# Performance work log

Hardware: AMD Instinct MI355X
Metric: run time of the kernel (lower is better)

## Reference

```python
import jax, jax.numpy as jnp
import numpy as np

N_NODES = 30000
N_EDGES = 300000
NUM_GRAPHS = 512
HID = 600
IN_FEATS = 9
NUM_TASKS = 128


def setup_inputs() -> dict:
    key = jax.random.key(0)
    ks = jax.random.split(key, 20)
    s = 0.05  # small init scale to keep activations bounded over 5 layers
    inp = {
        'x': jax.random.normal(ks[0], (N_NODES, IN_FEATS), jnp.float32),
        'edge_index': jax.random.randint(ks[1], (2, N_EDGES), 0, N_NODES, jnp.int64),
        'batch_ind': jnp.sort(jax.random.randint(ks[2], (N_NODES,), 0, NUM_GRAPHS, jnp.int64)),
        'w1_0': jax.random.normal(ks[3], (IN_FEATS, HID), jnp.float32) * s,
        'b1_0': jax.random.normal(ks[4], (HID,), jnp.float32) * s,
        'w2_0': jax.random.normal(ks[5], (HID, HID), jnp.float32) * s,
        'b2_0': jax.random.normal(ks[6], (HID,), jnp.float32) * s,
        'w1_r': jax.random.normal(ks[7], (4, HID, HID), jnp.float32) * s,
        'b1_r': jax.random.normal(ks[8], (4, HID), jnp.float32) * s,
        'w2_r': jax.random.normal(ks[9], (4, HID, HID), jnp.float32) * s,
        'b2_r': jax.random.normal(ks[10], (4, HID), jnp.float32) * s,
        'cw1': jax.random.normal(ks[11], (HID, 256), jnp.float32) * s,
        'cb1': jax.random.normal(ks[12], (256,), jnp.float32) * s,
        'cw2': jax.random.normal(ks[13], (256, 256), jnp.float32) * s,
        'cb2': jax.random.normal(ks[14], (256,), jnp.float32) * s,
        'cw3': jax.random.normal(ks[15], (256, NUM_TASKS), jnp.float32) * s,
        'cb3': jax.random.normal(ks[16], (NUM_TASKS,), jnp.float32) * s,
    }
    return inp


def _gin_conv(h, edge_index, w1, b1, w2, b2):
    # sum-aggregate neighbor features: messages flow src -> dst
    msgs = h[edge_index[0]]                                   # [E, d] gather
    agg = jax.ops.segment_sum(msgs, edge_index[1], num_segments=N_NODES)
    z = h + agg                                               # (1 + eps) * x + agg, eps = 0
    z = jax.nn.relu(z @ w1 + b1) @ w2 + b2                    # per-layer MLP [in, 600, 600]
    return z


def _forward(x, edge_index, batch_ind, w1_0, b1_0, w2_0, b2_0,
             w1_r, b1_r, w2_r, b2_r, cw1, cb1, cw2, cb2, cw3, cb3):
    h = _gin_conv(x, edge_index, w1_0, b1_0, w2_0, b2_0)
    h = jax.nn.relu(h)  # inter-layer activation (dropout is identity in eval)
    for i in range(4):  # layers 1..4 (fixed, structurally distinct params)
        h = _gin_conv(h, edge_index, w1_r[i], b1_r[i], w2_r[i], b2_r[i])
        if i < 3:
            h = jax.nn.relu(h)  # no act/dropout after final GNN layer (jk=None)
    feats = jax.ops.segment_sum(h, batch_ind, num_segments=NUM_GRAPHS)  # global_add_pool
    z = jax.nn.relu(feats @ cw1 + cb1)
    z = jax.nn.relu(z @ cw2 + cb2)
    return z @ cw3 + cb3  # [NUM_GRAPHS, NUM_TASKS]


def reference(x, edge_index, batch_ind, w1_0, b1_0, w2_0, b2_0,
              w1_r, b1_r, w2_r, b2_r, cw1, cb1, cw2, cb2, cw3, cb3):
    return _forward(x, edge_index, batch_ind, w1_0, b1_0, w2_0, b2_0,
                    w1_r, b1_r, w2_r, b2_r, cw1, cb1, cw2, cb2, cw3, cb3)
```

## Files before the change

### kernel.cpp

```cpp
#include <hip/hip_runtime.h>

#define N_NODES 30000
#define N_EDGES 300000
#define NUM_GRAPHS 512
#define HID 600
#define IN_FEATS 9
#define NUM_TASKS 128

#define MPAD 30080
#define HPAD 640
#define K0PAD 32

typedef __attribute__((ext_vector_type(4))) float f32x4;
typedef __attribute__((ext_vector_type(8))) short bf16x8;


__device__ __forceinline__ float bflo(unsigned int v) {
  union { unsigned int u; float f; } c; c.u = v << 16; return c.f;
}
__device__ __forceinline__ float bfhi(unsigned int v) {
  union { unsigned int u; float f; } c; c.u = v & 0xffff0000u; return c.f;
}
__device__ __forceinline__ unsigned short f2bf(float f) {
  union { float f; unsigned int u; } c; c.f = f;
  unsigned int u = c.u;
  return (unsigned short)((u + 0x7fffu + ((u >> 16) & 1u)) >> 16);
}
__device__ __forceinline__ unsigned int pack2(float a, float b) {
  return (unsigned int)f2bf(a) | ((unsigned int)f2bf(b) << 16);
}


__global__ void k_hist(const int* __restrict__ keys, int* __restrict__ counts, int n) {
  int i = blockIdx.x * blockDim.x + threadIdx.x;
  if (i < n) atomicAdd(&counts[keys[i]], 1);
}

__global__ __launch_bounds__(1024) void k_exscan(const int* __restrict__ in,
                                                 int* __restrict__ out,
                                                 int* cursor, int n) {
  __shared__ int buf[1024];
  int tid = threadIdx.x;
  int CH = (n + 1023) / 1024;
  int base = tid * CH;
  int s = 0;
  for (int j = 0; j < CH; ++j) {
    int i = base + j;
    if (i < n) s += in[i];
  }
  buf[tid] = s;
  __syncthreads();
  for (int off = 1; off < 1024; off <<= 1) {
    int t = (tid >= off) ? buf[tid - off] : 0;
    __syncthreads();
    buf[tid] += t;
    __syncthreads();
  }
  int pre = (tid == 0) ? 0 : buf[tid - 1];
  for (int j = 0; j < CH; ++j) {
    int i = base + j;
    if (i <= n) out[i] = pre;
    if (i < n) {
      int v = in[i];
      if (cursor) cursor[i] = pre;
      pre += v;
    }
  }
}

__global__ void k_scatter(const int* __restrict__ src, const int* __restrict__ dst,
                          int* __restrict__ cursor, int* __restrict__ edge_src, int E) {
  int e = blockIdx.x * blockDim.x + threadIdx.x;
  if (e < E) {
    int pos = atomicAdd(&cursor[dst[e]], 1);
    edge_src[pos] = src[e];
  }
}


__global__ void k_wt0(const float* __restrict__ w1_0, unsigned short* __restrict__ wt0) {
  int idx = blockIdx.x * 256 + threadIdx.x;
  if (idx >= HPAD * K0PAD) return;
  int n = idx / K0PAD, k = idx % K0PAD;
  float v = (n < HID && k < IN_FEATS) ? w1_0[(size_t)k * HID + n] : 0.f;
  wt0[idx] = f2bf(v);
}

__global__ __launch_bounds__(256) void k_wt_tiled(
    const float* __restrict__ w2_0, const float* __restrict__ w1_r,
    const float* __restrict__ w2_r, unsigned short* __restrict__ wts) {
  __shared__ float tile[64][65];
  int b = blockIdx.x;
  int w = b / 100;
  int tb = b % 100;
  int tn = (tb % 10) * 64;
  int tk = (tb / 10) * 64;
  const float* W;
  if (w == 0) W = w2_0;
  else if (w < 5) W = w1_r + (size_t)(w - 1) * HID * HID;
  else W = w2_r + (size_t)(w - 5) * HID * HID;
  int t = threadIdx.x;
  int lx = t & 63, ly = t >> 6;
#pragma unroll
  for (int i = 0; i < 16; ++i) {
    int k = tk + ly + i * 4;
    int n = tn + lx;
    float v = (k < HID && n < HID) ? W[(size_t)k * HID + n] : 0.f;
    tile[ly + i * 4][lx] = v;
  }
  __syncthreads();
  unsigned short* dst = wts + (size_t)w * HPAD * HPAD;
#pragma unroll
  for (int i = 0; i < 16; ++i) {
    int n = tn + ly + i * 4;
    int k = tk + lx;
    dst[(size_t)n * HPAD + k] = f2bf(tile[lx][ly + i * 4]);
  }
}

__global__ void k_bias_all(const float* __restrict__ b1_0, const float* __restrict__ b2_0,
                           const float* __restrict__ b1_r, const float* __restrict__ b2_r,
                           float* __restrict__ biases) {
  int idx = blockIdx.x * 256 + threadIdx.x;
  if (idx >= 10 * HPAD) return;
  int w = idx / HPAD, i = idx % HPAD;
  float v = 0.f;
  if (i < HID) {
    if (w == 0) v = b1_0[i];
    else if (w == 1) v = b2_0[i];
    else if (w < 6) v = b1_r[(size_t)(w - 2) * HID + i];
    else v = b2_r[(size_t)(w - 6) * HID + i];
  }
  biases[idx] = v;
}

__global__ void k_xconv(const float* __restrict__ x, unsigned short* __restrict__ xb) {
  int idx = blockIdx.x * 256 + threadIdx.x;
  if (idx >= MPAD * K0PAD) return;
  int m = idx >> 5, k = idx & 31;
  float v = (m < N_NODES && k < IN_FEATS) ? x[(size_t)m * IN_FEATS + k] : 0.f;
  xb[idx] = f2bf(v);
}


template <int U>
__global__ __launch_bounds__(256) void k_agg_bf16(
    const unsigned int* __restrict__ h, const int* __restrict__ ptr,
    const int* __restrict__ esrc, unsigned int* __restrict__ z, int n_nodes) {
  int wave = threadIdx.x >> 6, lane = threadIdx.x & 63;
  int node = blockIdx.x * 4 + wave;
  if (node >= n_nodes) return;
  int beg = ptr[node], end = ptr[node + 1];
  const unsigned int* hn = h + (size_t)node * U;
  float a0[5], a1[5];
#pragma unroll
  for (int i = 0; i < 5; ++i) {
    int u = lane + i * 64;
    if (u < U) { unsigned int v = hn[u]; a0[i] = bflo(v); a1[i] = bfhi(v); }
    else { a0[i] = 0.f; a1[i] = 0.f; }
  }
  int e = beg;
  for (; e + 2 <= end; e += 2) {
    const unsigned int* p0 = h + (size_t)esrc[e] * U;
    const unsigned int* p1 = h + (size_t)esrc[e + 1] * U;
    unsigned int v0[5], v1[5];
#pragma unroll
    for (int i = 0; i < 5; ++i) {
      int u = lane + i * 64;
      if (u < U) { v0[i] = p0[u]; v1[i] = p1[u]; }
      else { v0[i] = 0; v1[i] = 0; }
    }
#pragma unroll
    for (int i = 0; i < 5; ++i) {
      a0[i] += bflo(v0[i]) + bflo(v1[i]);
      a1[i] += bfhi(v0[i]) + bfhi(v1[i]);
    }
  }
  if (e < end) {
    const unsigned int* p0 = h + (size_t)esrc[e] * U;
#pragma unroll
    for (int i = 0; i < 5; ++i) {
      int u = lane + i * 64;
      if (u < U) { unsigned int v = p0[u]; a0[i] += bflo(v); a1[i] += bfhi(v); }
    }
  }
  unsigned int* zn = z + (size_t)node * U;
#pragma unroll
  for (int i = 0; i < 5; ++i) {
    int u = lane + i * 64;
    if (u < U) zn[u] = pack2(a0[i], a1[i]);
  }
}


__global__ __launch_bounds__(256) void k_pool_bf16(
    const unsigned int* __restrict__ h, const int* __restrict__ gptr,
    float* __restrict__ feats) {
  const int U = HPAD / 2;
  __shared__ float red[4][HPAD];
  int t = threadIdx.x;
  int wave = t >> 6, lane = t & 63;
  int g = blockIdx.x;
  int beg = gptr[g], end = gptr[g + 1];
  float a0[5] = {0.f, 0.f, 0.f, 0.f, 0.f}, a1[5] = {0.f, 0.f, 0.f, 0.f, 0.f};
  for (int i = beg + wave; i < end; i += 4) {
    const unsigned int* hi = h + (size_t)i * U;
#pragma unroll
    for (int j = 0; j < 5; ++j) {
      unsigned int v = hi[lane + j * 64];
      a0[j] += bflo(v); a1[j] += bfhi(v);
    }
  }
#pragma unroll
  for (int j = 0; j < 5; ++j) {
    int u = lane + j * 64;
    red[wave][2 * u] = a0[j];
    red[wave][2 * u + 1] = a1[j];
  }
  __syncthreads();
  float* fg = feats + (size_t)g * HPAD;
  for (int c = t; c < HPAD; c += 256)
    fg[c] = red[0][c] + red[1][c] + red[2][c] + red[3][c];
}


#define GLOAD(gptr, lptr)                                                            \
  __builtin_amdgcn_global_load_lds(                                                  \
      (const __attribute__((address_space(1))) unsigned int*)(gptr),                 \
      (__attribute__((address_space(3))) unsigned int*)(lptr), 16, 0, 0)

__global__ __launch_bounds__(256) void k_mgemm(
    const unsigned short* __restrict__ A, const unsigned short* __restrict__ Bt,
    const float* __restrict__ bias, unsigned short* __restrict__ C,
    int lda, int ldb, int ldc, int K, int relu, int gy) {
  int G = gridDim.x;
  int orig = blockIdx.x;
  int q = G >> 3, r = G & 7;
  int xcd = orig & 7, local = orig >> 3;
  int wgid = (xcd < r ? xcd * (q + 1) : r * (q + 1) + (xcd - r) * q) + local;
  int n0 = (wgid % gy) * 128;
  int m0 = (wgid / gy) * 128;

  __shared__ unsigned short As[2][128 * 32];
  __shared__ unsigned short Bs[2][128 * 32];
  int t = threadIdx.x;
  int lane = t & 63, wave = t >> 6;
  int wm = (wave >> 1) * 64, wn = (wave & 1) * 64;

  f32x4 acc[4][4] = {};

  int off0 = t * 8, off1 = t * 8 + 2048;
  int rm0 = off0 >> 5, rk0 = off0 & 31;
  int rm1 = off1 >> 5, rk1 = off1 & 31;

  const unsigned short* Ar0 = A + (size_t)(m0 + rm0) * lda + rk0;
  const unsigned short* Ar1 = A + (size_t)(m0 + rm1) * lda + rk1;
  const unsigned short* Br0 = Bt + (size_t)(n0 + rm0) * ldb + rk0;
  const unsigned short* Br1 = Bt + (size_t)(n0 + rm1) * ldb + rk1;

  GLOAD(Ar0, &As[0][off0]);
  GLOAD(Ar1, &As[0][off1]);
  GLOAD(Br0, &Bs[0][off0]);
  GLOAD(Br1, &Bs[0][off1]);
  asm volatile("s_waitcnt vmcnt(0)" ::: "memory");
  __builtin_amdgcn_s_barrier();

  int nt = K >> 5;
  int cur = 0;
  int kk = (lane >> 4) * 8;
  int ra = wm + (lane & 15);
  int rb = wn + (lane & 15);

  for (int tt = 0; tt < nt; ++tt) {
    if (tt + 1 < nt) {
      int k1 = (tt + 1) << 5;
      GLOAD(Ar0 + k1, &As[cur ^ 1][off0]);
      GLOAD(Ar1 + k1, &As[cur ^ 1][off1]);
      GLOAD(Br0 + k1, &Bs[cur ^ 1][off0]);
      GLOAD(Br1 + k1, &Bs[cur ^ 1][off1]);
    }
    bf16x8 a[4], b[4];
#pragma unroll
    for (int i = 0; i < 4; ++i)
      a[i] = *(const bf16x8*)(&As[cur][(ra + i * 16) * 32 + kk]);
#pragma unroll
    for (int j = 0; j < 4; ++j)
      b[j] = *(const bf16x8*)(&Bs[cur][(rb + j * 16) * 32 + kk]);
#pragma unroll
    for (int i = 0; i < 4; ++i)
#pragma unroll
      for (int j = 0; j < 4; ++j)
        acc[i][j] = __builtin_amdgcn_mfma_f32_16x16x32_bf16(a[i], b[j], acc[i][j], 0, 0, 0);
    asm volatile("s_waitcnt vmcnt(0)" ::: "memory");
    __builtin_amdgcn_s_barrier();
    cur ^= 1;
  }

  int col = lane & 15, r4 = (lane >> 4) * 4;
#pragma unroll
  for (int j = 0; j < 4; ++j) {
    int n = n0 + wn + j * 16 + col;
    float bv = bias[n];
#pragma unroll
    for (int i = 0; i < 4; ++i) {
      int mb = m0 + wm + i * 16 + r4;
#pragma unroll
      for (int rr = 0; rr < 4; ++rr) {
        float v = acc[i][j][rr] + bv;
        if (relu) v = fmaxf(v, 0.f);
        C[(size_t)(mb + rr) * ldc + n] = f2bf(v);
      }
    }
  }
}


__global__ __launch_bounds__(256) void k_classifier(
    const float* __restrict__ feats,
    const float* __restrict__ cw1, const float* __restrict__ cb1,
    const float* __restrict__ cw2, const float* __restrict__ cb2,
    const float* __restrict__ cw3, const float* __restrict__ cb3,
    float* __restrict__ out) {
  __shared__ float f[HID];
  __shared__ float red[4][256];
  __shared__ float z1[256];
  __shared__ float z2[256];
  int g = blockIdx.x;
  int t = threadIdx.x;
  int wave = t >> 6, lane = t & 63;
  for (int i = t; i < HID; i += 256) f[i] = feats[(size_t)g * HPAD + i];
  __syncthreads();

  {
    float acc[4] = {0.f, 0.f, 0.f, 0.f};
    int k0 = wave * 150, k1 = k0 + 150;
    for (int k = k0; k < k1; ++k) {
      float fv = f[k];
      const float* row = cw1 + (size_t)k * 256;
#pragma unroll
      for (int j = 0; j < 4; ++j) acc[j] += fv * row[lane + j * 64];
    }
#pragma unroll
    for (int j = 0; j < 4; ++j) red[wave][lane + j * 64] = acc[j];
  }
  __syncthreads();
  z1[t] = fmaxf(red[0][t] + red[1][t] + red[2][t] + red[3][t] + cb1[t], 0.f);
  __syncthreads();

  {
    float acc[4] = {0.f, 0.f, 0.f, 0.f};
    int k0 = wave * 64, k1 = k0 + 64;
    for (int k = k0; k < k1; ++k) {
      float zv = z1[k];
      const float* row = cw2 + (size_t)k * 256;
#pragma unroll
      for (int j = 0; j < 4; ++j) acc[j] += zv * row[lane + j * 64];
    }
    __syncthreads();
#pragma unroll
    for (int j = 0; j < 4; ++j) red[wave][lane + j * 64] = acc[j];
  }
  __syncthreads();
  z2[t] = fmaxf(red[0][t] + red[1][t] + red[2][t] + red[3][t] + cb2[t], 0.f);
  __syncthreads();

  {
    float a0 = 0.f, a1 = 0.f;
    int k0 = wave * 64, k1 = k0 + 64;
    for (int k = k0; k < k1; ++k) {
      float zv = z2[k];
      const float* row = cw3 + (size_t)k * NUM_TASKS;
      a0 += zv * row[lane];
      a1 += zv * row[lane + 64];
    }
    __syncthreads();
    red[wave][lane] = a0;
    red[wave][lane + 64] = a1;
  }
  __syncthreads();
  if (t < NUM_TASKS)
    out[(size_t)g * NUM_TASKS + t] = red[0][t] + red[1][t] + red[2][t] + red[3][t] + cb3[t];
}


extern "C" void kernel_launch(void* const* d_in, const int* in_sizes, int n_in,
                              void* d_out, int out_size, void* d_ws, size_t ws_size,
                              hipStream_t stream) {
  const float* x      = (const float*)d_in[0];
  const int*   ei     = (const int*)d_in[1];
  const int*   batch  = (const int*)d_in[2];
  const float* w1_0   = (const float*)d_in[3];
  const float* b1_0   = (const float*)d_in[4];
  const float* w2_0   = (const float*)d_in[5];
  const float* b2_0   = (const float*)d_in[6];
  const float* w1_r   = (const float*)d_in[7];
  const float* b1_r   = (const float*)d_in[8];
  const float* w2_r   = (const float*)d_in[9];
  const float* b2_r   = (const float*)d_in[10];
  const float* cw1    = (const float*)d_in[11];
  const float* cb1    = (const float*)d_in[12];
  const float* cw2    = (const float*)d_in[13];
  const float* cb2    = (const float*)d_in[14];
  const float* cw3    = (const float*)d_in[15];
  const float* cb3    = (const float*)d_in[16];
  float* out = (float*)d_out;

  const int* e_src = ei;
  const int* e_dst = ei + N_EDGES;

  const size_t HBUF = (size_t)MPAD * HPAD;
  const size_t ZBUF = (size_t)MPAD * K0PAD;
  const size_t WT   = (size_t)HPAD * HPAD;

  unsigned short* hA  = (unsigned short*)d_ws;
  unsigned short* hB  = hA + HBUF;
  unsigned short* hC  = hB + HBUF;
  unsigned short* z0  = hC + HBUF;
  unsigned short* xb  = z0 + ZBUF;
  unsigned short* wt0 = xb + ZBUF;
  unsigned short* wts = wt0 + (size_t)HPAD * K0PAD;
  float* biases = (float*)(wts + 9 * WT);
  float* feats  = biases + 10 * HPAD;
  int* row_ptr  = (int*)(feats + (size_t)NUM_GRAPHS * HPAD);
  int* counts   = row_ptr + (N_NODES + 1);
  int* edge_src = counts + N_NODES;
  int* gptr     = edge_src + N_EDGES;
  int* gcnt     = gptr + (NUM_GRAPHS + 1);

  k_wt0<<<(HPAD * K0PAD + 255) / 256, 256, 0, stream>>>(w1_0, wt0);
  k_wt_tiled<<<9 * 100, 256, 0, stream>>>(w2_0, w1_r, w2_r, wts);
  k_bias_all<<<(10 * HPAD + 255) / 256, 256, 0, stream>>>(b1_0, b2_0, b1_r, b2_r, biases);
  k_xconv<<<(MPAD * K0PAD + 255) / 256, 256, 0, stream>>>(x, xb);

  hipMemsetAsync(counts, 0, N_NODES * sizeof(int), stream);
  k_hist<<<(N_EDGES + 255) / 256, 256, 0, stream>>>(e_dst, counts, N_EDGES);
  k_exscan<<<1, 1024, 0, stream>>>(counts, row_ptr, counts, N_NODES);
  k_scatter<<<(N_EDGES + 255) / 256, 256, 0, stream>>>(e_src, e_dst, counts, edge_src, N_EDGES);

  hipMemsetAsync(gcnt, 0, NUM_GRAPHS * sizeof(int), stream);
  k_hist<<<(N_NODES + 255) / 256, 256, 0, stream>>>(batch, gcnt, N_NODES);
  k_exscan<<<1, 1024, 0, stream>>>(gcnt, gptr, nullptr, NUM_GRAPHS);

  const int G = (MPAD / 128) * (HPAD / 128);
  const int GY = HPAD / 128;

  k_agg_bf16<K0PAD / 2><<<(N_NODES + 3) / 4, 256, 0, stream>>>(
      (const unsigned int*)xb, row_ptr, edge_src, (unsigned int*)z0, N_NODES);
  k_mgemm<<<G, 256, 0, stream>>>(z0, wt0, biases + 0 * HPAD, hC, K0PAD, K0PAD, HPAD, K0PAD, 1, GY);
  k_mgemm<<<G, 256, 0, stream>>>(hC, wts, biases + 1 * HPAD, hA, HPAD, HPAD, HPAD, HPAD, 1, GY);

  unsigned short* h = hA;
  unsigned short* z = hB;
  unsigned short* tb = hC;
  for (int i = 0; i < 4; ++i) {
    k_agg_bf16<HPAD / 2><<<(N_NODES + 3) / 4, 256, 0, stream>>>(
        (const unsigned int*)h, row_ptr, edge_src, (unsigned int*)z, N_NODES);
    k_mgemm<<<G, 256, 0, stream>>>(z, wts + (1 + (size_t)i) * WT, biases + (2 + i) * HPAD, tb,
                                   HPAD, HPAD, HPAD, HPAD, 1, GY);
    k_mgemm<<<G, 256, 0, stream>>>(tb, wts + (5 + (size_t)i) * WT, biases + (6 + i) * HPAD, z,
                                   HPAD, HPAD, HPAD, HPAD, (i < 3) ? 1 : 0, GY);
    unsigned short* tmp = h; h = z; z = tmp;
  }

  k_pool_bf16<<<NUM_GRAPHS, 256, 0, stream>>>((const unsigned int*)h, gptr, feats);
  k_classifier<<<NUM_GRAPHS, 256, 0, stream>>>(feats, cw1, cb1, cw2, cb2, cw3, cb3, out);
}
```

Before: 821.1 us.

## Triple-buffer GEMM loads, unroll aggregation by four, parallelize CSR scan

```diff
diff --git a/kernel.cpp b/kernel.cpp
--- a/kernel.cpp
+++ b/kernel.cpp
@@ -65,6 +65,44 @@
       if (cursor) cursor[i] = pre;
       pre += v;
     }
+  }
+}
+
+__global__ __launch_bounds__(256) void k_scan1(const int* __restrict__ in,
+                                               int* __restrict__ partials, int n) {
+  __shared__ int buf[256];
+  int i = blockIdx.x * 256 + threadIdx.x;
+  buf[threadIdx.x] = (i < n) ? in[i] : 0;
+  __syncthreads();
+  for (int off = 128; off; off >>= 1) {
+    if (threadIdx.x < off) buf[threadIdx.x] += buf[threadIdx.x + off];
+    __syncthreads();
+  }
+  if (threadIdx.x == 0) partials[blockIdx.x] = buf[0];
+}
+
+__global__ __launch_bounds__(256) void k_scan3(const int* __restrict__ in,
+                                               const int* __restrict__ poff,
+                                               int* __restrict__ out,
+                                               int* __restrict__ cursor, int n) {
+  __shared__ int buf[256];
+  int b = blockIdx.x, t = threadIdx.x;
+  int i = b * 256 + t;
+  int v = (i < n) ? in[i] : 0;
+  buf[t] = v;
+  __syncthreads();
+  for (int off = 1; off < 256; off <<= 1) {
+    int x = (t >= off) ? buf[t - off] : 0;
+    __syncthreads();
+    buf[t] += x;
+    __syncthreads();
+  }
+  int base = poff[b];
+  int excl = base + buf[t] - v;
+  if (i < n) {
+    out[i] = excl;
+    cursor[i] = excl;
+    if (i == n - 1) out[n] = base + buf[t];
   }
 }
 
@@ -160,23 +198,25 @@
     else { a0[i] = 0.f; a1[i] = 0.f; }
   }
   int e = beg;
-  for (; e + 2 <= end; e += 2) {
+  for (; e + 4 <= end; e += 4) {
     const unsigned int* p0 = h + (size_t)esrc[e] * U;
     const unsigned int* p1 = h + (size_t)esrc[e + 1] * U;
-    unsigned int v0[5], v1[5];
+    const unsigned int* p2 = h + (size_t)esrc[e + 2] * U;
+    const unsigned int* p3 = h + (size_t)esrc[e + 3] * U;
+    unsigned int v0[5], v1[5], v2[5], v3[5];
 #pragma unroll
     for (int i = 0; i < 5; ++i) {
       int u = lane + i * 64;
-      if (u < U) { v0[i] = p0[u]; v1[i] = p1[u]; }
-      else { v0[i] = 0; v1[i] = 0; }
+      if (u < U) { v0[i] = p0[u]; v1[i] = p1[u]; v2[i] = p2[u]; v3[i] = p3[u]; }
+      else { v0[i] = 0; v1[i] = 0; v2[i] = 0; v3[i] = 0; }
     }
 #pragma unroll
     for (int i = 0; i < 5; ++i) {
-      a0[i] += bflo(v0[i]) + bflo(v1[i]);
-      a1[i] += bfhi(v0[i]) + bfhi(v1[i]);
-    }
-  }
-  if (e < end) {
+      a0[i] += (bflo(v0[i]) + bflo(v1[i])) + (bflo(v2[i]) + bflo(v3[i]));
+      a1[i] += (bfhi(v0[i]) + bfhi(v1[i])) + (bfhi(v2[i]) + bfhi(v3[i]));
+    }
+  }
+  for (; e < end; ++e) {
     const unsigned int* p0 = h + (size_t)esrc[e] * U;
 #pragma unroll
     for (int i = 0; i < 5; ++i) {
@@ -241,8 +281,8 @@
   int n0 = (wgid % gy) * 128;
   int m0 = (wgid / gy) * 128;
 
-  __shared__ unsigned short As[2][128 * 32];
-  __shared__ unsigned short Bs[2][128 * 32];
+  __shared__ unsigned short As[3][128 * 32];
+  __shared__ unsigned short Bs[3][128 * 32];
   int t = threadIdx.x;
   int lane = t & 63, wave = t >> 6;
   int wm = (wave >> 1) * 64, wn = (wave & 1) * 64;
@@ -258,26 +298,37 @@
   const unsigned short* Br0 = Bt + (size_t)(n0 + rm0) * ldb + rk0;
   const unsigned short* Br1 = Bt + (size_t)(n0 + rm1) * ldb + rk1;
 
+  int nt = K >> 5;
   GLOAD(Ar0, &As[0][off0]);
   GLOAD(Ar1, &As[0][off1]);
   GLOAD(Br0, &Bs[0][off0]);
   GLOAD(Br1, &Bs[0][off1]);
-  asm volatile("s_waitcnt vmcnt(0)" ::: "memory");
-  __builtin_amdgcn_s_barrier();
-
-  int nt = K >> 5;
-  int cur = 0;
+  if (nt > 1) {
+    GLOAD(Ar0 + 32, &As[1][off0]);
+    GLOAD(Ar1 + 32, &As[1][off1]);
+    GLOAD(Br0 + 32, &Bs[1][off0]);
+    GLOAD(Br1 + 32, &Bs[1][off1]);
+  }
+
   int kk = (lane >> 4) * 8;
   int ra = wm + (lane & 15);
   int rb = wn + (lane & 15);
+  int cur = 0;
 
   for (int tt = 0; tt < nt; ++tt) {
     if (tt + 1 < nt) {
-      int k1 = (tt + 1) << 5;
-      GLOAD(Ar0 + k1, &As[cur ^ 1][off0]);
-      GLOAD(Ar1 + k1, &As[cur ^ 1][off1]);
-      GLOAD(Br0 + k1, &Bs[cur ^ 1][off0]);
-      GLOAD(Br1 + k1, &Bs[cur ^ 1][off1]);
+      asm volatile("s_waitcnt vmcnt(4)" ::: "memory");
+    } else {
+      asm volatile("s_waitcnt vmcnt(0)" ::: "memory");
+    }
+    __builtin_amdgcn_s_barrier();
+    if (tt + 2 < nt) {
+      int k2 = (tt + 2) << 5;
+      int nb = cur + 2; if (nb >= 3) nb -= 3;
+      GLOAD(Ar0 + k2, &As[nb][off0]);
+      GLOAD(Ar1 + k2, &As[nb][off1]);
+      GLOAD(Br0 + k2, &Bs[nb][off0]);
+      GLOAD(Br1 + k2, &Bs[nb][off1]);
     }
     bf16x8 a[4], b[4];
 #pragma unroll
@@ -291,9 +342,7 @@
 #pragma unroll
       for (int j = 0; j < 4; ++j)
         acc[i][j] = __builtin_amdgcn_mfma_f32_16x16x32_bf16(a[i], b[j], acc[i][j], 0, 0, 0);
-    asm volatile("s_waitcnt vmcnt(0)" ::: "memory");
-    __builtin_amdgcn_s_barrier();
-    cur ^= 1;
+    cur += 1; if (cur >= 3) cur = 0;
   }
 
   int col = lane & 15, r4 = (lane >> 4) * 4;
@@ -411,6 +460,7 @@
   const size_t HBUF = (size_t)MPAD * HPAD;
   const size_t ZBUF = (size_t)MPAD * K0PAD;
   const size_t WT   = (size_t)HPAD * HPAD;
+  const int NB = (N_NODES + 255) / 256;
 
   unsigned short* hA  = (unsigned short*)d_ws;
   unsigned short* hB  = hA + HBUF;
@@ -426,6 +476,8 @@
   int* edge_src = counts + N_NODES;
   int* gptr     = edge_src + N_EDGES;
   int* gcnt     = gptr + (NUM_GRAPHS + 1);
+  int* partials = gcnt + NUM_GRAPHS;
+  int* poff     = partials + (NB + 1);
 
   k_wt0<<<(HPAD * K0PAD + 255) / 256, 256, 0, stream>>>(w1_0, wt0);
   k_wt_tiled<<<9 * 100, 256, 0, stream>>>(w2_0, w1_r, w2_r, wts);
@@ -434,7 +486,9 @@
 
   hipMemsetAsync(counts, 0, N_NODES * sizeof(int), stream);
   k_hist<<<(N_EDGES + 255) / 256, 256, 0, stream>>>(e_dst, counts, N_EDGES);
-  k_exscan<<<1, 1024, 0, stream>>>(counts, row_ptr, counts, N_NODES);
+  k_scan1<<<NB, 256, 0, stream>>>(counts, partials, N_NODES);
+  k_exscan<<<1, 1024, 0, stream>>>(partials, poff, nullptr, NB);
+  k_scan3<<<NB, 256, 0, stream>>>(counts, poff, row_ptr, counts, N_NODES);
   k_scatter<<<(N_EDGES + 255) / 256, 256, 0, stream>>>(e_src, e_dst, counts, edge_src, N_EDGES);
 
   hipMemsetAsync(gcnt, 0, NUM_GRAPHS * sizeof(int), stream);
```

Measured after the change: 761.9 us. 7.2% less time.
